# Optimization experiments

Measured on AMD Instinct MI355X. Metric: run time of the kernel, lower is better.

## Reference

```python
import jax, jax.numpy as jnp
import numpy as np

B, NQ, NK, D, H = 4, 2048, 2048, 1024, 16
HD = D // H


def setup_inputs() -> dict:
    key = jax.random.key(0)
    ks = jax.random.split(key, 11)
    s = 1.0 / np.sqrt(D)
    return {
        "q": jax.random.normal(ks[0], (B, NQ, D), jnp.float32),
        "k": jax.random.normal(ks[1], (B, NK, D), jnp.float32),
        "v": jax.random.normal(ks[2], (B, NK, D), jnp.float32),
        "Wq": jax.random.uniform(ks[3], (D, D), jnp.float32, -s, s),
        "bq": jax.random.uniform(ks[4], (D,), jnp.float32, -s, s),
        "Wk": jax.random.uniform(ks[5], (D, D), jnp.float32, -s, s),
        "bk": jax.random.uniform(ks[6], (D,), jnp.float32, -s, s),
        "Wv": jax.random.uniform(ks[7], (D, D), jnp.float32, -s, s),
        "bv": jax.random.uniform(ks[8], (D,), jnp.float32, -s, s),
        "Wo": jax.random.uniform(ks[9], (D, D), jnp.float32, -s, s),
        "bo": jax.random.uniform(ks[10], (D,), jnp.float32, -s, s),
    }


def reference(q, k, v, Wq, bq, Wk, bk, Wv, bv, Wo, bo):
    # Linear projections (torch Linear: x @ W.T + b), split into heads [B,H,N,HD]
    qh = (q @ Wq.T + bq).reshape(B, NQ, H, HD).transpose(0, 2, 1, 3)
    kh = (k @ Wk.T + bk).reshape(B, NK, H, HD).transpose(0, 2, 1, 3)
    vh = (v @ Wv.T + bv).reshape(B, NK, H, HD).transpose(0, 2, 1, 3)
    scores = jnp.einsum('bhqd,bhkd->bhqk', qh, kh) / np.sqrt(HD)  # [B,H,Nq,Nk]
    probs = jax.nn.softmax(scores, axis=-1)
    out = jnp.einsum('bhqk,bhkd->bhqd', probs, vh)
    out = out.transpose(0, 2, 1, 3).reshape(B, NQ, D)
    return out @ Wo.T + bo
```

## Files before the change

### kernel.cpp

```cpp
#include <hip/hip_runtime.h>
#include <hip/hip_bf16.h>
#include <cstdint>
#include <cstddef>


typedef __bf16 bf16x8 __attribute__((ext_vector_type(8)));
typedef float f32x4 __attribute__((ext_vector_type(4)));

#define BB 4
#define NQ 2048
#define NK 2048
#define DD 1024
#define HH 16
#define HD 64

#define QSCALE (0.125f * 1.4426950408889634f)

#if __has_builtin(__builtin_amdgcn_exp2f)
#define EXP2F(x) __builtin_amdgcn_exp2f(x)
#else
#define EXP2F(x) exp2f(x)
#endif

__device__ inline void gld_lds16(const void* g, void* lds) {
  __builtin_amdgcn_global_load_lds(
      (__attribute__((address_space(1))) unsigned int*)(g),
      (__attribute__((address_space(3))) unsigned int*)(lds),
      16, 0, 0);
}

__device__ inline bool probe_f32(const void* p) {
  const unsigned short* u = (const unsigned short*)p;
  int bad = 0;
#pragma unroll
  for (int i = 0; i < 64; ++i) {
    const int e = (u[2 * i] >> 7) & 0xFF;
    bad += (e > 0x8F) ? 1 : 0;
  }
  return bad >= 4;
}

__device__ inline bf16x8 cvt8(const float* src) {
  union { bf16x8 v; __hip_bfloat16 h[8]; } u;
#pragma unroll
  for (int j = 0; j < 8; ++j) u.h[j] = __float2bfloat16(src[j]);
  return u.v;
}

__global__ __launch_bounds__(256) void cvt_all(
    const void* __restrict__ q, const void* __restrict__ k,
    const void* __restrict__ v,
    const void* __restrict__ Wq, const void* __restrict__ Wk,
    const void* __restrict__ Wv, const void* __restrict__ Wo,
    __hip_bfloat16* __restrict__ qb, __hip_bfloat16* __restrict__ kb,
    __hip_bfloat16* __restrict__ vb, __hip_bfloat16* __restrict__ Wb) {
  const int bidx = blockIdx.x;
  const void* src; __hip_bfloat16* dst; size_t voff;
  if (bidx < 1536) {
    const int s = bidx >> 9;
    src = s == 0 ? q : (s == 1 ? k : v);
    dst = s == 0 ? qb : (s == 1 ? kb : vb);
    voff = (size_t)(bidx & 511) * 2048;
  } else {
    const int wi = (bidx - 1536) >> 6;
    src = wi == 0 ? Wq : (wi == 1 ? Wk : (wi == 2 ? Wv : Wo));
    dst = Wb + (size_t)wi * (DD * DD);
    voff = (size_t)((bidx - 1536) & 63) * 2048;
  }
  __shared__ int sflag;
  if (threadIdx.x == 0) sflag = probe_f32(src) ? 1 : 0;
  __syncthreads();
  const bool f32 = sflag != 0;
  const int t = threadIdx.x;
#pragma unroll
  for (int i = 0; i < 8; ++i) {
    const size_t j = voff + (size_t)i * 256 + t;
    if (f32) {
      union { f32x4 v2[2]; float f[8]; } u;
      const f32x4* s4 = (const f32x4*)src;
      u.v2[0] = s4[j * 2]; u.v2[1] = s4[j * 2 + 1];
      *(bf16x8*)(dst + j * 8) = cvt8(u.f);
    } else {
      *(f32x4*)(dst + j * 8) = ((const f32x4*)src)[j];
    }
  }
}

__global__ __launch_bounds__(256, 3) void gemm_fast(
    const __hip_bfloat16* __restrict__ qb, const __hip_bfloat16* __restrict__ kb,
    const __hip_bfloat16* __restrict__ vb, const __hip_bfloat16* __restrict__ At,
    const __hip_bfloat16* __restrict__ Wb,
    const void* __restrict__ bq, const void* __restrict__ bk,
    const void* __restrict__ bv, const void* __restrict__ bo,
    const void* __restrict__ WoOrig,
    void* __restrict__ Qp, void* __restrict__ Kp,
    void* __restrict__ Vt, void* __restrict__ Out, int cfg0) {
  __shared__ __align__(16) __hip_bfloat16 sA[128 * 64];
  __shared__ __align__(16) __hip_bfloat16 sB[128 * 64];
  const int t = threadIdx.x;
  const int wave = t >> 6, lane = t & 63;
  const int q4 = lane >> 4, c16 = lane & 15;
  const int xr = c16 & 7;
  const int wr = wave >> 1, wc = wave & 1;

  const int bid = blockIdx.x;
  const int xcd = bid & 7, idx = bid >> 3;
  const int z = idx >> 6;
  const int r6 = idx & 63;
  const int bm = xcd * 8 + (r6 >> 3);
  const int bn = r6 & 7;
  const int cfg = cfg0 + z;

  const __hip_bfloat16* A; const void* biasv; void* Cv; int mode; float scale = 1.f;
  if (cfg == 0)      { A = qb; biasv = bq; Cv = Qp; mode = 0; scale = QSCALE; }
  else if (cfg == 1) { A = kb; biasv = bk; Cv = Kp; mode = 0; }
  else if (cfg == 2) { A = vb; biasv = bv; Cv = Vt; mode = 1; }
  else               { A = At; biasv = bo; Cv = Out; mode = 2; }
  const __hip_bfloat16* Bm = Wb + (size_t)cfg * (DD * DD);

  const bool bias_f32 = probe_f32(biasv);
  const bool c_f32 = (mode == 2) && probe_f32(WoOrig);

  f32x4 acc[4][4];
#pragma unroll
  for (int i = 0; i < 4; ++i)
#pragma unroll
    for (int j = 0; j < 4; ++j) acc[i][j] = (f32x4){0.f, 0.f, 0.f, 0.f};

  const size_t baseA = (size_t)bm * 128 * DD;
  const size_t baseB = (size_t)bn * 128 * DD;

  size_t offA[4], offB[4];
  int lslot[4];
#pragma unroll
  for (int i = 0; i < 4; ++i) {
    const int slot = i * 256 + t;
    const int row = slot >> 3, pg = (slot & 7) ^ (row & 7);
    lslot[i] = slot;
    offA[i] = baseA + (size_t)row * DD + pg * 8;
    offB[i] = baseB + (size_t)row * DD + pg * 8;
  }

  for (int k0 = 0; k0 < DD; k0 += 64) {
    __syncthreads();
#pragma unroll
    for (int i = 0; i < 4; ++i)
      gld_lds16(A + offA[i] + k0, sA + lslot[i] * 8);
#pragma unroll
    for (int i = 0; i < 4; ++i)
      gld_lds16(Bm + offB[i] + k0, sB + lslot[i] * 8);
    __syncthreads();

#pragma unroll
    for (int ks = 0; ks < 2; ++ks) {
      bf16x8 af[4], bfm[4];
#pragma unroll
      for (int rt = 0; rt < 4; ++rt)
        af[rt] = *(const bf16x8*)(sA + (wr * 64 + rt * 16 + c16) * 64 +
                                  ((ks * 4 + q4) ^ xr) * 8);
#pragma unroll
      for (int ct = 0; ct < 4; ++ct)
        bfm[ct] = *(const bf16x8*)(sB + (wc * 64 + ct * 16 + c16) * 64 +
                                   ((ks * 4 + q4) ^ xr) * 8);
#pragma unroll
      for (int rt = 0; rt < 4; ++rt)
#pragma unroll
        for (int ct = 0; ct < 4; ++ct)
          acc[rt][ct] = __builtin_amdgcn_mfma_f32_16x16x32_bf16(af[rt], bfm[ct],
                                                                acc[rt][ct], 0, 0, 0);
    }
  }

  if (mode == 1) {
    __syncthreads();
    __hip_bfloat16* sT = wc ? sB : sA;
#pragma unroll
    for (int ct = 0; ct < 4; ++ct) {
      const int col = ct * 16 + c16;
      const int colg = bn * 128 + wc * 64 + col;
      const float bvx = bias_f32 ? ((const float*)biasv)[colg]
                                 : __bfloat162float(((const __hip_bfloat16*)biasv)[colg]);
      const int sw = (col & 7) << 3;
#pragma unroll
      for (int rt = 0; rt < 4; ++rt) {
        union { uint2 u; __hip_bfloat16 hx[4]; } pk;
#pragma unroll
        for (int r = 0; r < 4; ++r)
          pk.hx[r] = __float2bfloat16((acc[rt][ct][r] + bvx) * scale);
        const int rowl = wr * 64 + rt * 16 + q4 * 4;
        *(uint2*)(sT + col * 128 + (rowl ^ sw)) = pk.u;
      }
    }
    __syncthreads();
    const int bb = bm >> 4;
    const int kb0 = (bm & 15) * 128;
#pragma unroll
    for (int i = 0; i < 8; ++i) {
      const int idx2 = i * 256 + t;
      const int half = idx2 >> 10;
      const int rem = idx2 & 1023;
      const int col = rem >> 4;
      const int kc = rem & 15;
      const __hip_bfloat16* sTh = half ? sB : sA;
      bf16x8 vv = *(const bf16x8*)(sTh + col * 128 + ((kc * 8) ^ ((col & 7) << 3)));
      const int hh = bn * 2 + half;
      *(bf16x8*)((__hip_bfloat16*)Cv +
                 (size_t)((bb * HH + hh) * HD + col) * NK + kb0 + kc * 8) = vv;
    }
    return;
  }

  const int row0 = bm * 128 + wr * 64 + q4 * 4;
  const int col0 = bn * 128 + wc * 64 + c16;
#pragma unroll
  for (int ct = 0; ct < 4; ++ct) {
    const int col = col0 + ct * 16;
    const float bvx = bias_f32 ? ((const float*)biasv)[col]
                               : __bfloat162float(((const __hip_bfloat16*)biasv)[col]);
#pragma unroll
    for (int rt = 0; rt < 4; ++rt) {
#pragma unroll
      for (int r = 0; r < 4; ++r) {
        const int row = row0 + rt * 16 + r;
        const float val = (acc[rt][ct][r] + bvx) * scale;
        if (c_f32) {
          ((float*)Cv)[(size_t)row * DD + col] = val;
        } else {
          ((__hip_bfloat16*)Cv)[(size_t)row * DD + col] = __float2bfloat16(val);
        }
      }
    }
  }
}

__device__ inline void ld_slot(bool f32, const void* basep, size_t eoff,
                               f32x4& lo, f32x4& hi) {
  if (f32) {
    const f32x4* p = (const f32x4*)((const float*)basep + eoff);
    lo = p[0]; hi = p[1];
  } else {
    lo = *(const f32x4*)((const __hip_bfloat16*)basep + eoff);
  }
}

__device__ inline void st_slot(bool f32, __hip_bfloat16* dst, f32x4 lo, f32x4 hi) {
  if (f32) {
    union { f32x4 v[2]; float f[8]; } u;
    u.v[0] = lo; u.v[1] = hi;
    *(bf16x8*)dst = cvt8(u.f);
  } else {
    *(f32x4*)dst = lo;
  }
}

__global__ __launch_bounds__(256, 3) void gemm_mha(
    const void* __restrict__ qin, const void* __restrict__ kin,
    const void* __restrict__ vin, const void* __restrict__ ain,
    const void* __restrict__ Wq, const void* __restrict__ bq,
    const void* __restrict__ Wk, const void* __restrict__ bk,
    const void* __restrict__ Wv, const void* __restrict__ bv,
    const void* __restrict__ Wo, const void* __restrict__ bo,
    void* __restrict__ Qp, void* __restrict__ Kp,
    void* __restrict__ Vt, void* __restrict__ Out, int cfg0) {
  __shared__ __align__(16) __hip_bfloat16 sA[2][128 * 32];
  __shared__ __align__(16) __hip_bfloat16 sB[2][128 * 32];
  const int t = threadIdx.x;
  const int wave = t >> 6, lane = t & 63;
  const int q4 = lane >> 4, c16 = lane & 15;
  const int wr = wave >> 1, wc = wave & 1;

  const int bid = blockIdx.x;
  const int xcd = bid & 7, idx = bid >> 3;
  const int z = idx >> 6;
  const int r6 = idx & 63;
  const int bm = xcd * 8 + (r6 >> 3);
  const int bn = r6 & 7;
  const int cfg = cfg0 + z;

  const void *Av, *Bv, *biasv; void* Cv; int mode; float scale = 1.f;
  if (cfg == 0)      { Av = qin; Bv = Wq; biasv = bq; Cv = Qp; mode = 0; scale = QSCALE; }
  else if (cfg == 1) { Av = kin; Bv = Wk; biasv = bk; Cv = Kp; mode = 0; }
  else if (cfg == 2) { Av = vin; Bv = Wv; biasv = bv; Cv = Vt; mode = 1; }
  else               { Av = ain; Bv = Wo; biasv = bo; Cv = Out; mode = 2; }

  const bool a_f32 = probe_f32(Av);
  const bool b_f32 = probe_f32(Bv);
  const bool c_f32 = (mode == 2) && b_f32;

  f32x4 acc[4][4];
#pragma unroll
  for (int i = 0; i < 4; ++i)
#pragma unroll
    for (int j = 0; j < 4; ++j) acc[i][j] = (f32x4){0.f, 0.f, 0.f, 0.f};

  const size_t baseA = (size_t)bm * 128 * DD;
  const size_t baseB = (size_t)bn * 128 * DD;
  const int po = ((q4) ^ (c16 & 3)) * 8;

  size_t offA[2], offB[2];
  int lslot[2];
#pragma unroll
  for (int i = 0; i < 2; ++i) {
    const int slot = i * 256 + t;
    const int row = slot >> 2, pg = (slot & 3) ^ (row & 3);
    lslot[i] = slot;
    offA[i] = baseA + (size_t)row * DD + pg * 8;
    offB[i] = baseB + (size_t)row * DD + pg * 8;
  }

  f32x4 Alo[2], Ahi[2], Blo[2], Bhi[2];
#pragma unroll
  for (int i = 0; i < 2; ++i) {
    ld_slot(a_f32, Av, offA[i], Alo[i], Ahi[i]);
    ld_slot(b_f32, Bv, offB[i], Blo[i], Bhi[i]);
  }

  for (int k0 = 0, it = 0; k0 < DD; k0 += 32, ++it) {
    const int p = it & 1;
#pragma unroll
    for (int i = 0; i < 2; ++i) {
      st_slot(a_f32, &sA[p][lslot[i] * 8], Alo[i], Ahi[i]);
      st_slot(b_f32, &sB[p][lslot[i] * 8], Blo[i], Bhi[i]);
    }
    __syncthreads();

    if (k0 + 32 < DD) {
#pragma unroll
      for (int i = 0; i < 2; ++i) {
        ld_slot(a_f32, Av, offA[i] + k0 + 32, Alo[i], Ahi[i]);
        ld_slot(b_f32, Bv, offB[i] + k0 + 32, Blo[i], Bhi[i]);
      }
    }

    bf16x8 af[4], bfm[4];
#pragma unroll
    for (int rt = 0; rt < 4; ++rt)
      af[rt] = *(const bf16x8*)(&sA[p][0] + (wr * 64 + rt * 16 + c16) * 32 + po);
#pragma unroll
    for (int ct = 0; ct < 4; ++ct)
      bfm[ct] = *(const bf16x8*)(&sB[p][0] + (wc * 64 + ct * 16 + c16) * 32 + po);
#pragma unroll
    for (int rt = 0; rt < 4; ++rt)
#pragma unroll
      for (int ct = 0; ct < 4; ++ct)
        acc[rt][ct] = __builtin_amdgcn_mfma_f32_16x16x32_bf16(af[rt], bfm[ct],
                                                              acc[rt][ct], 0, 0, 0);
  }

  const int row0 = bm * 128 + wr * 64 + q4 * 4;
  const int col0 = bn * 128 + wc * 64 + c16;
#pragma unroll
  for (int ct = 0; ct < 4; ++ct) {
    const int col = col0 + ct * 16;
    const float bvx = b_f32 ? ((const float*)biasv)[col]
                            : __bfloat162float(((const __hip_bfloat16*)biasv)[col]);
#pragma unroll
    for (int rt = 0; rt < 4; ++rt) {
#pragma unroll
      for (int r = 0; r < 4; ++r) {
        const int row = row0 + rt * 16 + r;
        const float val = (acc[rt][ct][r] + bvx) * scale;
        if (mode == 1) {
          const int b = row >> 11, key = row & 2047;
          const int h = col >> 6, hd = col & 63;
          ((__hip_bfloat16*)Cv)[(size_t)((b * HH + h) * HD + hd) * NK + key] =
              __float2bfloat16(val);
        } else if (c_f32) {
          ((float*)Cv)[(size_t)row * DD + col] = val;
        } else {
          ((__hip_bfloat16*)Cv)[(size_t)row * DD + col] = __float2bfloat16(val);
        }
      }
    }
  }
}

__global__ __launch_bounds__(256, 4) void flash_attn(
    const __hip_bfloat16* Qp, const __hip_bfloat16* __restrict__ Kp,
    const __hip_bfloat16* __restrict__ Vt, __hip_bfloat16* Ao) {
  __shared__ __align__(16) __hip_bfloat16 sQP[128 * 64];
  __shared__ __align__(16) __hip_bfloat16 sK[2][64 * 64];
  __shared__ __align__(16) __hip_bfloat16 sV[64 * 64];

  const int t = threadIdx.x;
  const int wave = t >> 6, lane = t & 63;
  const int q4 = lane >> 4, c16 = lane & 15;
  const int xr = c16 & 7;

  const int bid = blockIdx.x;
  const int xcd = bid & 7, idx = bid >> 3;
  const int bh = xcd * 8 + (idx >> 4);
  const int qt = idx & 15;
  const int b = bh >> 4, h = bh & 15;

#pragma unroll
  for (int i = 0; i < 4; ++i) {
    const int slot = i * 256 + t;
    const int row = slot >> 3, pg = (slot & 7) ^ (row & 7);
    gld_lds16(Qp + ((size_t)(b * NQ + qt * 128 + row) * DD + h * 64 + pg * 8),
              sQP + slot * 8);
  }
#pragma unroll
  for (int i = 0; i < 2; ++i) {
    const int slot = i * 256 + t;
    const int row = slot >> 3, pg = (slot & 7) ^ (row & 7);
    gld_lds16(Kp + ((size_t)(b * NK + row) * DD + h * 64 + pg * 8),
              &sK[0][0] + slot * 8);
  }

  f32x4 o[2][4];
#pragma unroll
  for (int g = 0; g < 2; ++g)
#pragma unroll
    for (int i = 0; i < 4; ++i) o[g][i] = (f32x4){0.f, 0.f, 0.f, 0.f};
  f32x4 lacc[2];
  lacc[0] = (f32x4){0.f, 0.f, 0.f, 0.f};
  lacc[1] = (f32x4){0.f, 0.f, 0.f, 0.f};

  union { bf16x8 v; unsigned short u[8]; } one8;
#pragma unroll
  for (int j = 0; j < 8; ++j) one8.u[j] = 0x3F80;

  __syncthreads();

  bf16x8 aq[2][2];
#pragma unroll
  for (int qg = 0; qg < 2; ++qg)
#pragma unroll
    for (int ks = 0; ks < 2; ++ks)
      aq[qg][ks] = *(const bf16x8*)(sQP + (wave * 32 + qg * 16 + c16) * 64 +
                                    ((ks * 4 + q4) ^ xr) * 8);

  const int prow0 = wave * 32 + c16;
  const int prow1 = wave * 32 + 16 + c16;

  for (int kt = 0; kt < NK / 64; ++kt) {
    const int p = kt & 1;
#pragma unroll
    for (int i = 0; i < 2; ++i) {
      const int slot = i * 256 + t;
      const int row = slot >> 3, pg = (slot & 7) ^ (row & 7);
      gld_lds16(Vt + ((size_t)(bh * 64 + row) * NK + kt * 64 + pg * 8),
                &sV[0] + slot * 8);
    }
    if (kt + 1 < NK / 64) {
#pragma unroll
      for (int i = 0; i < 2; ++i) {
        const int slot = i * 256 + t;
        const int row = slot >> 3, pg = (slot & 7) ^ (row & 7);
        gld_lds16(Kp + ((size_t)(b * NK + (kt + 1) * 64 + row) * DD + h * 64 + pg * 8),
                  &sK[p ^ 1][0] + slot * 8);
      }
    }

    f32x4 s[2][4];
    __builtin_amdgcn_s_setprio(1);
#pragma unroll
    for (int ct = 0; ct < 4; ++ct) {
      bf16x8 bk0 = *(const bf16x8*)(&sK[p][0] + (ct * 16 + c16) * 64 + ((0 + q4) ^ xr) * 8);
      bf16x8 bk1 = *(const bf16x8*)(&sK[p][0] + (ct * 16 + c16) * 64 + ((4 + q4) ^ xr) * 8);
#pragma unroll
      for (int qg = 0; qg < 2; ++qg) {
        f32x4 z = (f32x4){0.f, 0.f, 0.f, 0.f};
        z = __builtin_amdgcn_mfma_f32_16x16x32_bf16(bk0, aq[qg][0], z, 0, 0, 0);
        z = __builtin_amdgcn_mfma_f32_16x16x32_bf16(bk1, aq[qg][1], z, 0, 0, 0);
        s[qg][ct] = z;
      }
    }
    __builtin_amdgcn_s_setprio(0);

#pragma unroll
    for (int qg = 0; qg < 2; ++qg) {
      const int prow = qg ? prow1 : prow0;
#pragma unroll
      for (int ct = 0; ct < 4; ++ct) {
        union { uint2 u; __hip_bfloat16 hx[4]; } pk;
#pragma unroll
        for (int r = 0; r < 4; ++r)
          pk.hx[r] = __float2bfloat16(EXP2F(s[qg][ct][r]));
        const int pc = (ct * 2 + (q4 >> 1)) ^ xr;
        *(uint2*)(sQP + prow * 64 + pc * 8 + (q4 & 1) * 4) = pk.u;
      }
    }

    __syncthreads();

    __builtin_amdgcn_s_setprio(1);
#pragma unroll
    for (int kk = 0; kk < 2; ++kk) {
      bf16x8 bvf[4];
#pragma unroll
      for (int ct2 = 0; ct2 < 4; ++ct2)
        bvf[ct2] = *(const bf16x8*)(&sV[0] + (ct2 * 16 + c16) * 64 + ((kk * 4 + q4) ^ xr) * 8);
      bf16x8 ap0 = *(const bf16x8*)(sQP + prow0 * 64 + ((kk * 4 + q4) ^ xr) * 8);
      bf16x8 ap1 = *(const bf16x8*)(sQP + prow1 * 64 + ((kk * 4 + q4) ^ xr) * 8);
      lacc[0] = __builtin_amdgcn_mfma_f32_16x16x32_bf16(ap0, one8.v, lacc[0], 0, 0, 0);
      lacc[1] = __builtin_amdgcn_mfma_f32_16x16x32_bf16(ap1, one8.v, lacc[1], 0, 0, 0);
#pragma unroll
      for (int ct2 = 0; ct2 < 4; ++ct2) {
        o[0][ct2] = __builtin_amdgcn_mfma_f32_16x16x32_bf16(ap0, bvf[ct2], o[0][ct2], 0, 0, 0);
        o[1][ct2] = __builtin_amdgcn_mfma_f32_16x16x32_bf16(ap1, bvf[ct2], o[1][ct2], 0, 0, 0);
      }
    }
    __builtin_amdgcn_s_setprio(0);

    __syncthreads();
  }

  float linv[2][4];
#pragma unroll
  for (int qg = 0; qg < 2; ++qg)
#pragma unroll
    for (int r = 0; r < 4; ++r) linv[qg][r] = 1.f / lacc[qg][r];

#pragma unroll
  for (int qg = 0; qg < 2; ++qg)
#pragma unroll
    for (int ct2 = 0; ct2 < 4; ++ct2)
#pragma unroll
      for (int r = 0; r < 4; ++r) {
        const size_t row = (size_t)(b * NQ + qt * 128 + wave * 32 + qg * 16 + q4 * 4 + r);
        Ao[row * DD + h * 64 + ct2 * 16 + c16] = __float2bfloat16(o[qg][ct2][r] * linv[qg][r]);
      }
}

extern "C" void kernel_launch(void* const* d_in, const int* in_sizes, int n_in,
                              void* d_out, int out_size, void* d_ws, size_t ws_size,
                              hipStream_t stream) {
  const void* q  = d_in[0];
  const void* k  = d_in[1];
  const void* v  = d_in[2];
  const void* Wq = d_in[3];
  const void* bq = d_in[4];
  const void* Wk = d_in[5];
  const void* bk = d_in[6];
  const void* Wv = d_in[7];
  const void* bv = d_in[8];
  const void* Wo = d_in[9];
  const void* bo = d_in[10];

  const size_t MP = (size_t)BB * NQ;
  const size_t MAT = MP * DD;
  __hip_bfloat16* Qp = (__hip_bfloat16*)d_ws;
  __hip_bfloat16* Vt = Qp + MAT;
  __hip_bfloat16* Kp = (__hip_bfloat16*)d_out;
  __hip_bfloat16* At = Qp;

  const size_t NEED = (4 * MAT + 4 * (size_t)(DD * DD)) * sizeof(__hip_bfloat16);
  if (ws_size >= NEED) {
    __hip_bfloat16* kb = Vt + MAT;
    __hip_bfloat16* vb = kb + MAT;
    __hip_bfloat16* Wb = vb + MAT;
    __hip_bfloat16* qb = (__hip_bfloat16*)d_out + MAT;

    cvt_all<<<dim3(1792), 256, 0, stream>>>(q, k, v, Wq, Wk, Wv, Wo,
                                            qb, kb, vb, Wb);
    gemm_fast<<<dim3(1536), 256, 0, stream>>>(qb, kb, vb, At, Wb,
                                              bq, bk, bv, bo, Wo,
                                              Qp, Kp, Vt, d_out, 0);
    flash_attn<<<dim3(1024), 256, 0, stream>>>(Qp, Kp, Vt, At);
    gemm_fast<<<dim3(512), 256, 0, stream>>>(qb, kb, vb, At, Wb,
                                             bq, bk, bv, bo, Wo,
                                             Qp, Kp, Vt, d_out, 3);
  } else {
    gemm_mha<<<dim3(1536), 256, 0, stream>>>(
        q, k, v, At, Wq, bq, Wk, bk, Wv, bv, Wo, bo, Qp, Kp, Vt, d_out, 0);
    flash_attn<<<dim3(1024), 256, 0, stream>>>(Qp, Kp, Vt, At);
    gemm_mha<<<dim3(512), 256, 0, stream>>>(
        q, k, v, At, Wq, bq, Wk, bk, Wv, bv, Wo, bo, Qp, Kp, Vt, d_out, 3);
  }
}
```

Measured before the change: 330.9 us.

## Triple-buffer projection GEMM with 256x128 tiles and 512-thread blocks

```diff
diff --git a/kernel.cpp b/kernel.cpp
--- a/kernel.cpp
+++ b/kernel.cpp
@@ -86,7 +86,11 @@
   }
 }
 
-__global__ __launch_bounds__(256, 3) void gemm_fast(
+#define ABUF (256 * 64)
+#define BBUF (128 * 64)
+#define BUFSZ (ABUF + BBUF)
+
+__global__ __launch_bounds__(512, 2) void gemm_fast(
     const __hip_bfloat16* __restrict__ qb, const __hip_bfloat16* __restrict__ kb,
     const __hip_bfloat16* __restrict__ vb, const __hip_bfloat16* __restrict__ At,
     const __hip_bfloat16* __restrict__ Wb,
@@ -95,8 +99,7 @@
     const void* __restrict__ WoOrig,
     void* __restrict__ Qp, void* __restrict__ Kp,
     void* __restrict__ Vt, void* __restrict__ Out, int cfg0) {
-  __shared__ __align__(16) __hip_bfloat16 sA[128 * 64];
-  __shared__ __align__(16) __hip_bfloat16 sB[128 * 64];
+  __shared__ __align__(16) __hip_bfloat16 sm[3 * BUFSZ];
   const int t = threadIdx.x;
   const int wave = t >> 6, lane = t & 63;
   const int q4 = lane >> 4, c16 = lane & 15;
@@ -105,10 +108,10 @@
 
   const int bid = blockIdx.x;
   const int xcd = bid & 7, idx = bid >> 3;
-  const int z = idx >> 6;
-  const int r6 = idx & 63;
-  const int bm = xcd * 8 + (r6 >> 3);
-  const int bn = r6 & 7;
+  const int z = idx >> 5;
+  const int r5 = idx & 31;
+  const int bm = xcd * 4 + (r5 >> 3);
+  const int bn = r5 & 7;
   const int cfg = cfg0 + z;
 
   const __hip_bfloat16* A; const void* biasv; void* Cv; int mode; float scale = 1.f;
@@ -127,57 +130,89 @@
 #pragma unroll
     for (int j = 0; j < 4; ++j) acc[i][j] = (f32x4){0.f, 0.f, 0.f, 0.f};
 
-  const size_t baseA = (size_t)bm * 128 * DD;
+  const size_t baseA = (size_t)bm * 256 * DD;
   const size_t baseB = (size_t)bn * 128 * DD;
 
-  size_t offA[4], offB[4];
-  int lslot[4];
+  size_t offA[4], offB[2];
+  int slA[4], slB[2];
 #pragma unroll
   for (int i = 0; i < 4; ++i) {
-    const int slot = i * 256 + t;
+    const int slot = i * 512 + t;
     const int row = slot >> 3, pg = (slot & 7) ^ (row & 7);
-    lslot[i] = slot;
+    slA[i] = slot;
     offA[i] = baseA + (size_t)row * DD + pg * 8;
+  }
+#pragma unroll
+  for (int i = 0; i < 2; ++i) {
+    const int slot = i * 512 + t;
+    const int row = slot >> 3, pg = (slot & 7) ^ (row & 7);
+    slB[i] = slot;
     offB[i] = baseB + (size_t)row * DD + pg * 8;
   }
 
-  for (int k0 = 0; k0 < DD; k0 += 64) {
-    __syncthreads();
-#pragma unroll
-    for (int i = 0; i < 4; ++i)
-      gld_lds16(A + offA[i] + k0, sA + lslot[i] * 8);
-#pragma unroll
-    for (int i = 0; i < 4; ++i)
-      gld_lds16(Bm + offB[i] + k0, sB + lslot[i] * 8);
-    __syncthreads();
-
-#pragma unroll
-    for (int ks = 0; ks < 2; ++ks) {
-      bf16x8 af[4], bfm[4];
-#pragma unroll
-      for (int rt = 0; rt < 4; ++rt)
-        af[rt] = *(const bf16x8*)(sA + (wr * 64 + rt * 16 + c16) * 64 +
-                                  ((ks * 4 + q4) ^ xr) * 8);
-#pragma unroll
-      for (int ct = 0; ct < 4; ++ct)
-        bfm[ct] = *(const bf16x8*)(sB + (wc * 64 + ct * 16 + c16) * 64 +
-                                   ((ks * 4 + q4) ^ xr) * 8);
-#pragma unroll
-      for (int rt = 0; rt < 4; ++rt)
-#pragma unroll
-        for (int ct = 0; ct < 4; ++ct)
-          acc[rt][ct] = __builtin_amdgcn_mfma_f32_16x16x32_bf16(af[rt], bfm[ct],
-                                                                acc[rt][ct], 0, 0, 0);
+#define STAGE_TILE(bb, koff)                                          \
+  {                                                                   \
+    __hip_bfloat16* dA = sm + (bb) * BUFSZ;                           \
+    __hip_bfloat16* dB = dA + ABUF;                                   \
+    _Pragma("unroll")                                                 \
+    for (int i = 0; i < 4; ++i)                                       \
+      gld_lds16(A + offA[i] + (koff), dA + slA[i] * 8);               \
+    _Pragma("unroll")                                                 \
+    for (int i = 0; i < 2; ++i)                                       \
+      gld_lds16(Bm + offB[i] + (koff), dB + slB[i] * 8);              \
+  }
+
+#define COMPUTE_TILE(bb)                                              \
+  {                                                                   \
+    const __hip_bfloat16* cA = sm + (bb) * BUFSZ;                     \
+    const __hip_bfloat16* cB = cA + ABUF;                             \
+    _Pragma("unroll")                                                 \
+    for (int ks = 0; ks < 2; ++ks) {                                  \
+      bf16x8 af[4], bfm[4];                                           \
+      _Pragma("unroll")                                               \
+      for (int rt = 0; rt < 4; ++rt)                                  \
+        af[rt] = *(const bf16x8*)(cA + (wr * 64 + rt * 16 + c16) * 64 \
+                                  + ((ks * 4 + q4) ^ xr) * 8);        \
+      _Pragma("unroll")                                               \
+      for (int ct = 0; ct < 4; ++ct)                                  \
+        bfm[ct] = *(const bf16x8*)(cB + (wc * 64 + ct * 16 + c16) * 64\
+                                   + ((ks * 4 + q4) ^ xr) * 8);       \
+      _Pragma("unroll")                                               \
+      for (int rt = 0; rt < 4; ++rt)                                  \
+        _Pragma("unroll")                                             \
+        for (int ct = 0; ct < 4; ++ct)                                \
+          acc[rt][ct] = __builtin_amdgcn_mfma_f32_16x16x32_bf16(      \
+              af[rt], bfm[ct], acc[rt][ct], 0, 0, 0);                 \
+    }                                                                 \
+  }
+
+  STAGE_TILE(0, 0);
+  STAGE_TILE(1, 64);
+  asm volatile("s_waitcnt vmcnt(6)" ::: "memory");
+  __builtin_amdgcn_s_barrier();
+  __builtin_amdgcn_sched_barrier(0);
+
+#pragma unroll
+  for (int tt = 0; tt < 16; ++tt) {
+    if (tt + 2 < 16) STAGE_TILE((tt + 2) % 3, (tt + 2) * 64);
+    __builtin_amdgcn_s_setprio(1);
+    COMPUTE_TILE(tt % 3);
+    __builtin_amdgcn_s_setprio(0);
+    if (tt + 1 < 16) {
+      if (tt + 2 < 16) asm volatile("s_waitcnt vmcnt(6)" ::: "memory");
+      else             asm volatile("s_waitcnt vmcnt(0)" ::: "memory");
+      __builtin_amdgcn_s_barrier();
+      __builtin_amdgcn_sched_barrier(0);
     }
   }
 
   if (mode == 1) {
     __syncthreads();
-    __hip_bfloat16* sT = wc ? sB : sA;
+    __hip_bfloat16* sT = sm;
 #pragma unroll
     for (int ct = 0; ct < 4; ++ct) {
-      const int col = ct * 16 + c16;
-      const int colg = bn * 128 + wc * 64 + col;
+      const int col = wc * 64 + ct * 16 + c16;
+      const int colg = bn * 128 + col;
       const float bvx = bias_f32 ? ((const float*)biasv)[colg]
                                  : __bfloat162float(((const __hip_bfloat16*)biasv)[colg]);
       const int sw = (col & 7) << 3;
@@ -188,29 +223,27 @@
         for (int r = 0; r < 4; ++r)
           pk.hx[r] = __float2bfloat16((acc[rt][ct][r] + bvx) * scale);
         const int rowl = wr * 64 + rt * 16 + q4 * 4;
-        *(uint2*)(sT + col * 128 + (rowl ^ sw)) = pk.u;
+        *(uint2*)(sT + col * 256 + (rowl ^ sw)) = pk.u;
       }
     }
     __syncthreads();
-    const int bb = bm >> 4;
-    const int kb0 = (bm & 15) * 128;
+    const int bbat = bm >> 3;
+    const int kb0 = (bm & 7) * 256;
 #pragma unroll
     for (int i = 0; i < 8; ++i) {
-      const int idx2 = i * 256 + t;
-      const int half = idx2 >> 10;
-      const int rem = idx2 & 1023;
-      const int col = rem >> 4;
-      const int kc = rem & 15;
-      const __hip_bfloat16* sTh = half ? sB : sA;
-      bf16x8 vv = *(const bf16x8*)(sTh + col * 128 + ((kc * 8) ^ ((col & 7) << 3)));
-      const int hh = bn * 2 + half;
+      const int idx2 = i * 512 + t;
+      const int col = idx2 >> 5;
+      const int kc = idx2 & 31;
+      bf16x8 vv = *(const bf16x8*)(sT + col * 256 + ((kc * 8) ^ ((col & 7) << 3)));
+      const int hh = bn * 2 + (col >> 6);
+      const int hd = col & 63;
       *(bf16x8*)((__hip_bfloat16*)Cv +
-                 (size_t)((bb * HH + hh) * HD + col) * NK + kb0 + kc * 8) = vv;
+                 (size_t)((bbat * HH + hh) * HD + hd) * NK + kb0 + kc * 8) = vv;
     }
     return;
   }
 
-  const int row0 = bm * 128 + wr * 64 + q4 * 4;
+  const int row0 = bm * 256 + wr * 64 + q4 * 4;
   const int col0 = bn * 128 + wc * 64 + c16;
 #pragma unroll
   for (int ct = 0; ct < 4; ++ct) {
@@ -232,6 +265,8 @@
     }
   }
 }
+#undef STAGE_TILE
+#undef COMPUTE_TILE
 
 __device__ inline void ld_slot(bool f32, const void* basep, size_t eoff,
                                f32x4& lo, f32x4& hi) {
@@ -555,11 +590,11 @@
 
     cvt_all<<<dim3(1792), 256, 0, stream>>>(q, k, v, Wq, Wk, Wv, Wo,
                                             qb, kb, vb, Wb);
-    gemm_fast<<<dim3(1536), 256, 0, stream>>>(qb, kb, vb, At, Wb,
-                                              bq, bk, bv, bo, Wo,
-                                              Qp, Kp, Vt, d_out, 0);
+    gemm_fast<<<dim3(768), 512, 0, stream>>>(qb, kb, vb, At, Wb,
+                                             bq, bk, bv, bo, Wo,
+                                             Qp, Kp, Vt, d_out, 0);
     flash_attn<<<dim3(1024), 256, 0, stream>>>(Qp, Kp, Vt, At);
-    gemm_fast<<<dim3(512), 256, 0, stream>>>(qb, kb, vb, At, Wb,
+    gemm_fast<<<dim3(256), 512, 0, stream>>>(qb, kb, vb, At, Wb,
                                              bq, bk, bv, bo, Wo,
                                              Qp, Kp, Vt, d_out, 3);
   } else {
```

Result: faster. 315.7 us (-4.6%).
